# Optimization experiments

Hardware: AMD Instinct MI355X
Metric: run time of the kernel (lower is better)

## Reference

```python
import jax, jax.numpy as jnp
import numpy as np

H, DK, DV, BS = 8, 64, 64, 128


def setup_inputs() -> dict:
    key = jax.random.key(0)
    ks = jax.random.split(key, 6)
    B, T, D = 2, 8193, 1024
    inner = H * DK
    x = jax.random.normal(ks[0], (B, T, D), jnp.float32)
    s = 0.02
    Wq = jax.random.normal(ks[1], (D, inner), jnp.float32) * s
    Wk = jax.random.normal(ks[2], (D, inner), jnp.float32) * s
    Wv = jax.random.normal(ks[3], (D, H * DV), jnp.float32) * s
    Wo = jax.random.normal(ks[4], (H * DV, D), jnp.float32) * s
    bo = jnp.zeros((D,), jnp.float32)
    return {"x": x, "Wq": Wq, "Wk": Wk, "Wv": Wv, "Wo": Wo, "bo": bo}


def _bigbird(x, Wq, Wk, Wv, Wo, bo):
    B, T, D = x.shape
    N = T - 1
    nb = N // BS
    scale = 1.0 / jnp.sqrt(jnp.asarray(DK, x.dtype))
    # projections -> (B, H, T, d)
    q = (x @ Wq).reshape(B, T, H, DK).transpose(0, 2, 1, 3)
    k = (x @ Wk).reshape(B, T, H, DK).transpose(0, 2, 1, 3)
    v = (x @ Wv).reshape(B, T, H, DV).transpose(0, 2, 1, 3)

    # global token (position 0) attends to everything
    sg = jnp.einsum('bhd,bhtd->bht', q[:, :, 0], k) * scale
    pg = jax.nn.softmax(sg, axis=-1)
    out_g = jnp.einsum('bht,bhtd->bhd', pg, v)  # (B,H,DV)

    kg = k[:, :, 0]  # (B,H,DK)
    vg = v[:, :, 0]  # (B,H,DV)
    qx = q[:, :, 1:].reshape(B, H, nb, BS, DK)
    kx = k[:, :, 1:].reshape(B, H, nb, BS, DK)
    vx = v[:, :, 1:].reshape(B, H, nb, BS, DV)

    # zero-pad one block on each side (faithful to original: zero blocks, not masked)
    kp = jnp.pad(kx, ((0, 0), (0, 0), (1, 1), (0, 0), (0, 0)))
    vp = jnp.pad(vx, ((0, 0), (0, 0), (1, 1), (0, 0), (0, 0)))
    k_local = jnp.concatenate([kp[:, :, 0:nb], kp[:, :, 1:nb + 1], kp[:, :, 2:nb + 2]], axis=3)
    v_local = jnp.concatenate([vp[:, :, 0:nb], vp[:, :, 1:nb + 1], vp[:, :, 2:nb + 2]], axis=3)

    kg_e = jnp.broadcast_to(kg[:, :, None, None, :], (B, H, nb, 1, DK))
    vg_e = jnp.broadcast_to(vg[:, :, None, None, :], (B, H, nb, 1, DV))
    k_full = jnp.concatenate([kg_e, k_local], axis=3)  # (B,H,nb,1+3BS,DK)
    v_full = jnp.concatenate([vg_e, v_local], axis=3)

    scores = jnp.einsum('bhnqd,bhnkd->bhnqk', qx, k_full) * scale
    p = jax.nn.softmax(scores, axis=-1)
    out_x = jnp.einsum('bhnqk,bhnkd->bhnqd', p, v_full).reshape(B, H, N, DV)

    out = jnp.concatenate([out_g[:, :, None, :], out_x], axis=2)  # (B,H,T,DV)
    out = out.transpose(0, 2, 1, 3).reshape(B, T, H * DV)
    return out @ Wo + bo


def reference(x, Wq, Wk, Wv, Wo, bo):
    return _bigbird(x, Wq, Wk, Wv, Wo, bo)
```

## Files before the change

### kernel.cpp

```cpp
#include <hip/hip_runtime.h>
#include <hip/hip_bf16.h>

#define T_TOK 8193
#define MROWS 16386
#define NBLK  64
#define GCH   16
#define GCS   513

typedef __attribute__((ext_vector_type(8))) short bf16x8;
typedef __attribute__((ext_vector_type(4))) float f32x4;
typedef unsigned short u16;
typedef unsigned int   u32;

__device__ __forceinline__ float blo(u32 u){ return __uint_as_float(u << 16); }
__device__ __forceinline__ float bhi(u32 u){ return __uint_as_float(u & 0xffff0000u); }
__device__ __forceinline__ u16 f2b(float f){
  u32 u = __float_as_uint(f);
  u = (u + 0x7fffu + ((u >> 16) & 1u)) >> 16;
  return (u16)u;
}
__device__ __forceinline__ float b2f(u16 v){ return __uint_as_float(((u32)v) << 16); }

#define GLDS16(gsrc, ldst) \
  __builtin_amdgcn_global_load_lds((const __attribute__((address_space(1))) void*)(gsrc), \
                                   (__attribute__((address_space(3))) void*)(ldst), 16, 0, 0)

__global__ __launch_bounds__(256)
void convx(const float* __restrict__ x, u16* __restrict__ xb)
{
  const size_t i = (size_t)blockIdx.x * 256 + threadIdx.x;
  const float4* p = (const float4*)x + i * 2;
  float4 a = p[0], b = p[1];
  uint4 st;
  st.x = (u32)f2b(a.x) | ((u32)f2b(a.y) << 16);
  st.y = (u32)f2b(a.z) | ((u32)f2b(a.w) << 16);
  st.z = (u32)f2b(b.x) | ((u32)f2b(b.y) << 16);
  st.w = (u32)f2b(b.z) | ((u32)f2b(b.w) << 16);
  *(uint4*)(xb + i * 8) = st;
}

__global__ __launch_bounds__(256)
void transposeW(const float* __restrict__ B0, const float* __restrict__ B1,
                const float* __restrict__ B2, int bpart,
                u16* __restrict__ outT, int K)
{
  __shared__ float tile[64][65];
  const int n0 = blockIdx.x * 64;
  const int k0 = blockIdx.y * 64;
  const int tx = threadIdx.x & 63;
  const int ty = threadIdx.x >> 6;
  const int part = n0 / bpart;
  const float* Bm = part == 0 ? B0 : (part == 1 ? B1 : B2);
  const int bn = n0 - part * bpart;
  #pragma unroll
  for (int i = 0; i < 16; ++i) {
    int k = i * 4 + ty;
    tile[tx][k] = Bm[(size_t)(k0 + k) * bpart + bn + tx];
  }
  __syncthreads();
  #pragma unroll
  for (int i = 0; i < 16; ++i) {
    int r = i * 4 + ty;
    outT[(size_t)(n0 + r) * K + k0 + tx] = f2b(tile[r][tx]);
  }
}

template<bool OUT_F32>
__global__ __launch_bounds__(256)
void gemm_bf(const u16* __restrict__ A, const u16* __restrict__ BT,
             void* __restrict__ Cp, const float* __restrict__ bias,
             int M, int K, int ntm, int ntn, int ldc)
{
  __shared__ u16 As[128 * 32];
  __shared__ u16 Bs[128 * 32];
  const int tid  = threadIdx.x;
  const int lane = tid & 63;
  const int wid  = tid >> 6;
  const int l15  = lane & 15;
  const int g    = lane >> 4;
  const int wr   = (wid >> 1) * 64;
  const int wc   = (wid & 1) * 64;

  const int nwg  = gridDim.x;
  const int orig = blockIdx.x;
  const int q8 = nwg >> 3, r8 = nwg & 7;
  const int xcd = orig & 7, loc = orig >> 3;
  const int wg = (xcd < r8 ? xcd * (q8 + 1) : r8 * (q8 + 1) + (xcd - r8) * q8) + loc;
  const int GT  = 8;
  const int gsz = GT * ntn;
  const int tg  = wg / gsz;
  const int rem = wg - tg * gsz;
  const int gt  = (ntm - tg * GT < GT) ? (ntm - tg * GT) : GT;
  const int tn  = rem / gt;
  const int tml = rem - tn * gt;
  const int tm  = tg * GT + tml;
  const int bm0 = tm * 128, bn0 = tn * 128;

  f32x4 acc[4][4];
  #pragma unroll
  for (int i = 0; i < 4; ++i)
    #pragma unroll
    for (int j = 0; j < 4; ++j) { f32x4 z = {0.f,0.f,0.f,0.f}; acc[i][j] = z; }

  const int c0 = tid, c1 = tid + 256;
  int ar0 = bm0 + (c0 >> 2); if (ar0 >= M) ar0 = M - 1;
  int ar1 = bm0 + (c1 >> 2); if (ar1 >= M) ar1 = M - 1;
  const u16* Ag0 = A + (size_t)ar0 * K + (c0 & 3) * 8;
  const u16* Ag1 = A + (size_t)ar1 * K + (c1 & 3) * 8;
  const u16* Bg0 = BT + (size_t)(bn0 + (c0 >> 2)) * K + (c0 & 3) * 8;
  const u16* Bg1 = BT + (size_t)(bn0 + (c1 >> 2)) * K + (c1 & 3) * 8;
  u16* la0 = As + c0 * 8;  u16* la1 = As + c1 * 8;
  u16* lb0 = Bs + c0 * 8;  u16* lb1 = Bs + c1 * 8;

  for (int kt = 0; kt < K; kt += 32) {
    __syncthreads();
    GLDS16(Ag0 + kt, la0);
    GLDS16(Ag1 + kt, la1);
    GLDS16(Bg0 + kt, lb0);
    GLDS16(Bg1 + kt, lb1);
    __syncthreads();
    bf16x8 af[4], bfr[4];
    #pragma unroll
    for (int mi = 0; mi < 4; ++mi)
      af[mi] = *(const bf16x8*)&As[(wr + mi * 16 + l15) * 32 + g * 8];
    #pragma unroll
    for (int ni = 0; ni < 4; ++ni)
      bfr[ni] = *(const bf16x8*)&Bs[(wc + ni * 16 + l15) * 32 + g * 8];
    #pragma unroll
    for (int mi = 0; mi < 4; ++mi)
      #pragma unroll
      for (int ni = 0; ni < 4; ++ni)
        acc[mi][ni] = __builtin_amdgcn_mfma_f32_16x16x32_bf16(af[mi], bfr[ni], acc[mi][ni], 0, 0, 0);
  }

  const int r0 = g * 4;
  #pragma unroll
  for (int mi = 0; mi < 4; ++mi) {
    #pragma unroll
    for (int r = 0; r < 4; ++r) {
      int grow = bm0 + wr + mi * 16 + r0 + r;
      if (grow >= M) continue;
      #pragma unroll
      for (int ni = 0; ni < 4; ++ni) {
        int gcol  = bn0 + wc + ni * 16 + l15;
        float val = acc[mi][ni][r];
        if (OUT_F32) ((float*)Cp)[(size_t)grow * ldc + gcol] = val + bias[gcol];
        else         ((u16*)Cp)[(size_t)grow * ldc + gcol]   = f2b(val);
      }
    }
  }
}

__global__ __launch_bounds__(256)
void gsplit(const u16* __restrict__ qkv, float* __restrict__ gbuf)
{
  const int c   = blockIdx.x & 15;
  const int h   = (blockIdx.x >> 4) & 7;
  const int b   = blockIdx.x >> 7;
  const int tid = threadIdx.x;
  const int lane = tid & 63;
  const int wid  = tid >> 6;
  const int t0 = c * GCS;
  const int t1 = (t0 + GCS < T_TOK) ? (t0 + GCS) : T_TOK;
  const int nt = t1 - t0;

  __shared__ float sc[GCS];
  __shared__ float q0s[64];
  __shared__ float wredm[4], wreds[4];
  __shared__ float psum[4][64];

  const size_t base = (size_t)b * T_TOK * 1536;
  if (tid < 32) {
    u32 u = ((const u32*)(qkv + base + h * 64))[tid];
    q0s[2 * tid] = blo(u); q0s[2 * tid + 1] = bhi(u);
  }
  __syncthreads();

  float lmax = -INFINITY;
  for (int tt = tid; tt < nt; tt += 256) {
    const uint4* kp = (const uint4*)(qkv + base + (size_t)(t0 + tt) * 1536 + 512 + h * 64);
    float a = 0.f;
    #pragma unroll
    for (int q8 = 0; q8 < 8; ++q8) {
      uint4 kk = kp[q8];
      a += q0s[q8*8+0]*blo(kk.x) + q0s[q8*8+1]*bhi(kk.x)
         + q0s[q8*8+2]*blo(kk.y) + q0s[q8*8+3]*bhi(kk.y)
         + q0s[q8*8+4]*blo(kk.z) + q0s[q8*8+5]*bhi(kk.z)
         + q0s[q8*8+6]*blo(kk.w) + q0s[q8*8+7]*bhi(kk.w);
    }
    a *= 0.125f;
    sc[tt] = a;
    lmax = fmaxf(lmax, a);
  }
  for (int o = 32; o; o >>= 1) lmax = fmaxf(lmax, __shfl_xor(lmax, o, 64));
  if (lane == 0) wredm[wid] = lmax;
  __syncthreads();
  float bmax = fmaxf(fmaxf(wredm[0], wredm[1]), fmaxf(wredm[2], wredm[3]));
  float lsum = 0.f;
  for (int tt = tid; tt < nt; tt += 256) {
    float e = __expf(sc[tt] - bmax);
    sc[tt] = e;
    lsum += e;
  }
  for (int o = 32; o; o >>= 1) lsum += __shfl_xor(lsum, o, 64);
  if (lane == 0) wreds[wid] = lsum;
  __syncthreads();
  float bsum = wreds[0] + wreds[1] + wreds[2] + wreds[3];

  const int g = tid >> 6;
  const int d = tid & 63;
  float acc = 0.f;
  for (int tt = g; tt < nt; tt += 4)
    acc += sc[tt] * b2f(qkv[base + (size_t)(t0 + tt) * 1536 + 1024 + h * 64 + d]);
  psum[g][d] = acc;
  __syncthreads();

  float* rec = gbuf + ((size_t)(b * 8 + h) * GCH + c) * 66;
  if (tid < 64)
    rec[2 + tid] = psum[0][tid] + psum[1][tid] + psum[2][tid] + psum[3][tid];
  if (tid == 64) { rec[0] = bmax; rec[1] = bsum; }
}

__global__ __launch_bounds__(64)
void gmerge(const float* __restrict__ gbuf, u16* __restrict__ attnb)
{
  const int bh = blockIdx.x;
  const int d  = threadIdx.x;
  const float* recs = gbuf + (size_t)bh * GCH * 66;
  float m = -INFINITY;
  #pragma unroll
  for (int c = 0; c < GCH; ++c) m = fmaxf(m, recs[c * 66]);
  float l = 0.f, o = 0.f;
  #pragma unroll
  for (int c = 0; c < GCH; ++c) {
    float e = __expf(recs[c * 66] - m);
    l += recs[c * 66 + 1] * e;
    o += recs[c * 66 + 2 + d] * e;
  }
  const int b = bh >> 3, h = bh & 7;
  attnb[(size_t)b * T_TOK * 512 + h * 64 + d] = f2b(o / l);
}

__global__ __launch_bounds__(256)
void local_attn_mfma(const u16* __restrict__ qkv, u16* __restrict__ attnb)
{
  const int bid = blockIdx.x;
  const int n = bid & 63;
  const int h = (bid >> 6) & 7;
  const int b = bid >> 9;
  const int tid  = threadIdx.x;
  const int lane = tid & 63;
  const int wid  = tid >> 6;
  const int l15  = lane & 15;
  const int g    = lane >> 4;

  __shared__ u16 K_lds[128 * 72];
  __shared__ u16 V_T[64 * 136];
  __shared__ u16 P_lds[4][32 * 72];
  __shared__ float bb[4][2][32];
  __shared__ float Kg[64], Vg[64];

  const size_t rb = (size_t)b * T_TOK;
  if (tid < 64) {
    Kg[tid] = b2f(qkv[rb * 1536 + 512 + h * 64 + tid]);
    Vg[tid] = b2f(qkv[rb * 1536 + 1024 + h * 64 + tid]);
  }

  const int q0row = 1 + n * 128 + wid * 32;
  bf16x8 qf[2][2];
  #pragma unroll
  for (int qt = 0; qt < 2; ++qt)
    #pragma unroll
    for (int kk = 0; kk < 2; ++kk)
      qf[qt][kk] = *(const bf16x8*)(qkv + (rb + q0row + qt * 16 + l15) * 1536 + h * 64 + kk * 32 + g * 8);

  __syncthreads();

  float sg[2];
  #pragma unroll
  for (int qt = 0; qt < 2; ++qt) {
    float part = 0.f;
    #pragma unroll
    for (int kk = 0; kk < 2; ++kk)
      #pragma unroll
      for (int i = 0; i < 8; ++i)
        part += b2f((u16)qf[qt][kk][i]) * Kg[kk * 32 + g * 8 + i];
    part += __shfl_xor(part, 16, 64);
    part += __shfl_xor(part, 32, 64);
    sg[qt] = part * 0.125f;
  }

  float m[2] = {-INFINITY, -INFINITY};
  float l[2] = {0.f, 0.f};
  f32x4 of[2][4];
  #pragma unroll
  for (int qt = 0; qt < 2; ++qt)
    #pragma unroll
    for (int dt = 0; dt < 4; ++dt) { f32x4 z = {0.f,0.f,0.f,0.f}; of[qt][dt] = z; }

  for (int dblk = 0; dblk < 3; ++dblk) {
    const int blk = n + dblk - 1;
    if (blk < 0 || blk >= NBLK) continue;
    const size_t krow0 = rb + 1 + (size_t)blk * 128;

    __syncthreads();
    #pragma unroll
    for (int it = 0; it < 4; ++it) {
      int c = it * 256 + tid;
      int key = c >> 3, oct = c & 7;
      *(uint4*)&K_lds[key * 72 + oct * 8] =
          *(const uint4*)(qkv + (krow0 + key) * 1536 + 512 + h * 64 + oct * 8);
    }
    #pragma unroll
    for (int it = 0; it < 2; ++it) {
      int c = it * 256 + tid;
      int kp2 = c & 63, oct = c >> 6;
      const u16* s0 = qkv + (krow0 + 2 * kp2) * 1536 + 1024 + h * 64 + oct * 8;
      uint4 va = *(const uint4*)s0;
      uint4 vb4 = *(const uint4*)(s0 + 1536);
      union { uint4 q; u16 hh[8]; } ua, ub;
      ua.q = va; ub.q = vb4;
      #pragma unroll
      for (int i = 0; i < 8; ++i) {
        u32 w = (u32)ua.hh[i] | ((u32)ub.hh[i] << 16);
        *(u32*)&V_T[(oct * 8 + i) * 136 + 2 * kp2] = w;
      }
    }
    __syncthreads();

    f32x4 st[2][8];
    #pragma unroll
    for (int kt = 0; kt < 8; ++kt) {
      bf16x8 kfr[2];
      #pragma unroll
      for (int kk = 0; kk < 2; ++kk)
        kfr[kk] = *(const bf16x8*)&K_lds[(kt * 16 + l15) * 72 + kk * 32 + g * 8];
      #pragma unroll
      for (int qt = 0; qt < 2; ++qt) {
        f32x4 z = {0.f,0.f,0.f,0.f};
        z = __builtin_amdgcn_mfma_f32_16x16x32_bf16(kfr[0], qf[qt][0], z, 0, 0, 0);
        z = __builtin_amdgcn_mfma_f32_16x16x32_bf16(kfr[1], qf[qt][1], z, 0, 0, 0);
        st[qt][kt] = z;
      }
    }
    #pragma unroll
    for (int qt = 0; qt < 2; ++qt) {
      float bm = -INFINITY;
      #pragma unroll
      for (int kt = 0; kt < 8; ++kt)
        #pragma unroll
        for (int r = 0; r < 4; ++r) bm = fmaxf(bm, st[qt][kt][r]);
      bm = fmaxf(bm, __shfl_xor(bm, 16, 64));
      bm = fmaxf(bm, __shfl_xor(bm, 32, 64));
      bm *= 0.125f;
      float mn = fmaxf(m[qt], bm);
      float corr = __expf(m[qt] - mn);
      float bsum = 0.f;
      #pragma unroll
      for (int kt = 0; kt < 8; ++kt)
        #pragma unroll
        for (int r = 0; r < 4; ++r) {
          float p = __expf(__builtin_fmaf(st[qt][kt][r], 0.125f, -mn));
          st[qt][kt][r] = p;
          bsum += p;
        }
      bsum += __shfl_xor(bsum, 16, 64);
      bsum += __shfl_xor(bsum, 32, 64);
      l[qt] = l[qt] * corr + bsum;
      m[qt] = mn;
      if (lane < 16) bb[wid][0][qt * 16 + lane] = corr;
    }
    float rc[2][4];
    #pragma unroll
    for (int qt = 0; qt < 2; ++qt)
      #pragma unroll
      for (int r = 0; r < 4; ++r) rc[qt][r] = bb[wid][0][qt * 16 + g * 4 + r];
    #pragma unroll
    for (int qt = 0; qt < 2; ++qt)
      #pragma unroll
      for (int dt = 0; dt < 4; ++dt)
        #pragma unroll
        for (int r = 0; r < 4; ++r) of[qt][dt][r] *= rc[qt][r];

    u16* P_w = (u16*)P_lds[wid];
    #pragma unroll
    for (int half = 0; half < 2; ++half) {
      #pragma unroll
      for (int qt = 0; qt < 2; ++qt)
        #pragma unroll
        for (int k4 = 0; k4 < 4; ++k4) {
          int kt = half * 4 + k4;
          u16 h0 = f2b(st[qt][kt][0]), h1 = f2b(st[qt][kt][1]);
          u16 h2 = f2b(st[qt][kt][2]), h3 = f2b(st[qt][kt][3]);
          uint2 pk = { (u32)h0 | ((u32)h1 << 16), (u32)h2 | ((u32)h3 << 16) };
          *(uint2*)&P_w[(qt * 16 + l15) * 72 + k4 * 16 + g * 4] = pk;
        }
      #pragma unroll
      for (int ks = 0; ks < 2; ++ks) {
        bf16x8 pa[2];
        #pragma unroll
        for (int qt = 0; qt < 2; ++qt)
          pa[qt] = *(const bf16x8*)&P_w[(qt * 16 + l15) * 72 + ks * 32 + g * 8];
        #pragma unroll
        for (int dt = 0; dt < 4; ++dt) {
          bf16x8 vb = *(const bf16x8*)&V_T[(dt * 16 + l15) * 136 + half * 64 + ks * 32 + g * 8];
          #pragma unroll
          for (int qt = 0; qt < 2; ++qt)
            of[qt][dt] = __builtin_amdgcn_mfma_f32_16x16x32_bf16(pa[qt], vb, of[qt][dt], 0, 0, 0);
        }
      }
    }
  }

  const int nz = (n == 0) + (n == NBLK - 1);
  #pragma unroll
  for (int qt = 0; qt < 2; ++qt) {
    float mf   = fmaxf(m[qt], sg[qt]);
    float corr = __expf(m[qt] - mf);
    float eg   = __expf(sg[qt] - mf);
    float lf   = l[qt] * corr + eg;
    if (nz) lf += (float)(nz * 128) * __expf(-mf);
    float inv = 1.f / lf;
    if (lane < 16) {
      bb[wid][0][qt * 16 + lane] = corr * inv;
      bb[wid][1][qt * 16 + lane] = eg * inv;
    }
  }
  float vgr[4];
  #pragma unroll
  for (int dt = 0; dt < 4; ++dt) vgr[dt] = Vg[dt * 16 + l15];
  #pragma unroll
  for (int qt = 0; qt < 2; ++qt)
    #pragma unroll
    for (int r = 0; r < 4; ++r) {
      float af = bb[wid][0][qt * 16 + g * 4 + r];
      float bf = bb[wid][1][qt * 16 + g * 4 + r];
      int row = q0row + qt * 16 + g * 4 + r;
      u16* dst = attnb + (rb + row) * 512 + h * 64;
      #pragma unroll
      for (int dt = 0; dt < 4; ++dt)
        dst[dt * 16 + l15] = f2b(of[qt][dt][r] * af + bf * vgr[dt]);
    }
}

extern "C" void kernel_launch(void* const* d_in, const int* in_sizes, int n_in,
                              void* d_out, int out_size, void* d_ws, size_t ws_size,
                              hipStream_t stream) {
  (void)in_sizes; (void)n_in; (void)out_size; (void)ws_size;
  const float* x  = (const float*)d_in[0];
  const float* Wq = (const float*)d_in[1];
  const float* Wk = (const float*)d_in[2];
  const float* Wv = (const float*)d_in[3];
  const float* Wo = (const float*)d_in[4];
  const float* bo = (const float*)d_in[5];
  float* out = (float*)d_out;

  char* ws = (char*)d_ws;
  u16* qkv   = (u16*)ws;
  u16* xb    = (u16*)(ws + 50337792);
  u16* attnb = (u16*)(ws + 50337792);
  u16* WoT   = (u16*)(ws + 67117056);
  u16* WqkvT = (u16*)d_out;
  float* gbuf = (float*)((char*)d_out + (4 << 20));

  dim3 blk(256);
  convx<<<dim3(8193), blk, 0, stream>>>(x, xb);
  transposeW<<<dim3(24, 16), blk, 0, stream>>>(Wq, Wk, Wv, 512, WqkvT, 1024);
  gemm_bf<false><<<dim3(129 * 12), blk, 0, stream>>>(xb, WqkvT, qkv, nullptr, MROWS, 1024, 129, 12, 1536);
  transposeW<<<dim3(16, 8), blk, 0, stream>>>(Wo, Wo, Wo, 1024, WoT, 512);
  gsplit<<<dim3(256), blk, 0, stream>>>(qkv, gbuf);
  gmerge<<<dim3(16), dim3(64), 0, stream>>>(gbuf, attnb);
  local_attn_mfma<<<dim3(1024), blk, 0, stream>>>(qkv, attnb);
  gemm_bf<true><<<dim3(129 * 8), blk, 0, stream>>>(attnb, WoT, out, bo, MROWS, 512, 129, 8, 1024);
}
```

Measured before the change: 227.7 us.

## Triple-buffer GEMM LDS tiles with async prefetch and XOR-swizzled layout

The bf16 GEMM main loop now uses three LDS buffers and prefetches tiles two steps ahead with global_load_lds, waiting on vmcnt counts instead of a full sync after each load. This overlaps global-to-LDS traffic with the MFMA work. It also XOR-swizzles the 16-byte chunk positions in LDS so fragment reads hit fewer bank conflicts. In exchange it triples LDS use per block, which may lower occupancy, and the hand-written vmcnt waits depend on the exact number of outstanding loads.

Result: faster. 217.7 us (-4.4%).

```diff
diff --git a/kernel.cpp b/kernel.cpp
--- a/kernel.cpp
+++ b/kernel.cpp
@@ -71,8 +71,8 @@
              void* __restrict__ Cp, const float* __restrict__ bias,
              int M, int K, int ntm, int ntn, int ldc)
 {
-  __shared__ u16 As[128 * 32];
-  __shared__ u16 Bs[128 * 32];
+  __shared__ u16 As[3][128 * 32];
+  __shared__ u16 Bs[3][128 * 32];
   const int tid  = threadIdx.x;
   const int lane = tid & 63;
   const int wid  = tid >> 6;
@@ -102,36 +102,57 @@
     #pragma unroll
     for (int j = 0; j < 4; ++j) { f32x4 z = {0.f,0.f,0.f,0.f}; acc[i][j] = z; }
 
-  const int c0 = tid, c1 = tid + 256;
-  int ar0 = bm0 + (c0 >> 2); if (ar0 >= M) ar0 = M - 1;
-  int ar1 = bm0 + (c1 >> 2); if (ar1 >= M) ar1 = M - 1;
-  const u16* Ag0 = A + (size_t)ar0 * K + (c0 & 3) * 8;
-  const u16* Ag1 = A + (size_t)ar1 * K + (c1 & 3) * 8;
-  const u16* Bg0 = BT + (size_t)(bn0 + (c0 >> 2)) * K + (c0 & 3) * 8;
-  const u16* Bg1 = BT + (size_t)(bn0 + (c1 >> 2)) * K + (c1 & 3) * 8;
-  u16* la0 = As + c0 * 8;  u16* la1 = As + c1 * 8;
-  u16* lb0 = Bs + c0 * 8;  u16* lb1 = Bs + c1 * 8;
-
-  for (int kt = 0; kt < K; kt += 32) {
-    __syncthreads();
-    GLDS16(Ag0 + kt, la0);
-    GLDS16(Ag1 + kt, la1);
-    GLDS16(Bg0 + kt, lb0);
-    GLDS16(Bg1 + kt, lb1);
-    __syncthreads();
+  const int srcq = ((tid & 3) ^ ((tid >> 3) & 3)) * 8;
+  int ar0 = bm0 + (tid >> 2);      if (ar0 >= M) ar0 = M - 1;
+  int ar1 = bm0 + 64 + (tid >> 2); if (ar1 >= M) ar1 = M - 1;
+  const u16* Ag0 = A + (size_t)ar0 * K + srcq;
+  const u16* Ag1 = A + (size_t)ar1 * K + srcq;
+  const u16* Bg0 = BT + (size_t)(bn0 + (tid >> 2)) * K + srcq;
+  const u16* Bg1 = BT + (size_t)(bn0 + 64 + (tid >> 2)) * K + srcq;
+  const int ld0 = tid * 8, ld1 = tid * 8 + 2048;
+
+#define STAGE_T(bf, kt) do { \
+    GLDS16(Ag0 + (kt), &As[bf][ld0]); \
+    GLDS16(Ag1 + (kt), &As[bf][ld1]); \
+    GLDS16(Bg0 + (kt), &Bs[bf][ld0]); \
+    GLDS16(Bg1 + (kt), &Bs[bf][ld1]); \
+  } while (0)
+
+  const int Tst = K >> 5;
+  STAGE_T(0, 0);
+  STAGE_T(1, 32);
+
+  const int qa = (g ^ ((l15 >> 1) & 3)) * 8;
+
+  int cur = 0;
+  for (int t = 0; t < Tst; ++t) {
+    __builtin_amdgcn_s_barrier();
+    int nb = cur + 2; if (nb >= 3) nb -= 3;
+    if (t + 2 < Tst) {
+      STAGE_T(nb, (t + 2) * 32);
+      asm volatile("s_waitcnt vmcnt(8)" ::: "memory");
+    } else if (t + 2 == Tst) {
+      asm volatile("s_waitcnt vmcnt(4)" ::: "memory");
+    } else {
+      asm volatile("s_waitcnt vmcnt(0)" ::: "memory");
+    }
+    __builtin_amdgcn_s_barrier();
+    __builtin_amdgcn_sched_barrier(0);
     bf16x8 af[4], bfr[4];
     #pragma unroll
     for (int mi = 0; mi < 4; ++mi)
-      af[mi] = *(const bf16x8*)&As[(wr + mi * 16 + l15) * 32 + g * 8];
+      af[mi] = *(const bf16x8*)&As[cur][(wr + mi * 16 + l15) * 32 + qa];
     #pragma unroll
     for (int ni = 0; ni < 4; ++ni)
-      bfr[ni] = *(const bf16x8*)&Bs[(wc + ni * 16 + l15) * 32 + g * 8];
+      bfr[ni] = *(const bf16x8*)&Bs[cur][(wc + ni * 16 + l15) * 32 + qa];
     #pragma unroll
     for (int mi = 0; mi < 4; ++mi)
       #pragma unroll
       for (int ni = 0; ni < 4; ++ni)
         acc[mi][ni] = __builtin_amdgcn_mfma_f32_16x16x32_bf16(af[mi], bfr[ni], acc[mi][ni], 0, 0, 0);
-  }
+    cur = (cur + 1 == 3) ? 0 : cur + 1;
+  }
+#undef STAGE_T
 
   const int r0 = g * 4;
   #pragma unroll
```

## Replace GEMM with 256x256-tile, 8-wave, double-buffered, swizzled-LDS pipelined kernel

Applied to the files above, without the earlier changes.

Replaces the simple 128x128 single-buffered bf16 GEMM with a 256x256-tile kernel using 8 waves and a 128 KB double-buffered LDS ring. The LDS layout is XOR-swizzled, and loads for future k-slices are interleaved with MFMA phases using explicit vmcnt waits, barriers and setprio. The aim is to hide global-load latency and improve data reuse in both the QKV and output projections. In exchange it uses far more LDS and registers, and the grid has fewer workgroups (390 and 260), which risks tail imbalance.

Measured after the change: 205.1 us. -9.9%, faster.

```diff
diff --git a/kernel.cpp b/kernel.cpp
--- a/kernel.cpp
+++ b/kernel.cpp
@@ -66,79 +66,133 @@
 }
 
 template<bool OUT_F32>
-__global__ __launch_bounds__(256)
-void gemm_bf(const u16* __restrict__ A, const u16* __restrict__ BT,
-             void* __restrict__ Cp, const float* __restrict__ bias,
-             int M, int K, int ntm, int ntn, int ldc)
+__global__ __launch_bounds__(512, 2)
+void gemm8(const u16* __restrict__ A, const u16* __restrict__ BT,
+           void* __restrict__ Cp, const float* __restrict__ bias,
+           int M, int K, int ntm, int ntn, int ldc)
 {
-  __shared__ u16 As[128 * 32];
-  __shared__ u16 Bs[128 * 32];
+  __shared__ u16 lds[65536];
   const int tid  = threadIdx.x;
   const int lane = tid & 63;
   const int wid  = tid >> 6;
   const int l15  = lane & 15;
   const int g    = lane >> 4;
-  const int wr   = (wid >> 1) * 64;
-  const int wc   = (wid & 1) * 64;
+  const int wrh  = wid >> 2;
+  const int wc   = (wid & 3) * 64;
+  const int bh   = (wid & 3) >> 1;
+  const int wcl  = (wid & 1) * 64;
 
   const int nwg  = gridDim.x;
   const int orig = blockIdx.x;
   const int q8 = nwg >> 3, r8 = nwg & 7;
   const int xcd = orig & 7, loc = orig >> 3;
   const int wg = (xcd < r8 ? xcd * (q8 + 1) : r8 * (q8 + 1) + (xcd - r8) * q8) + loc;
-  const int GT  = 8;
+  const int GT  = 4;
   const int gsz = GT * ntn;
   const int tg  = wg / gsz;
   const int rem = wg - tg * gsz;
   const int gt  = (ntm - tg * GT < GT) ? (ntm - tg * GT) : GT;
   const int tn  = rem / gt;
   const int tml = rem - tn * gt;
-  const int tm  = tg * GT + tml;
-  const int bm0 = tm * 128, bn0 = tn * 128;
-
-  f32x4 acc[4][4];
-  #pragma unroll
-  for (int i = 0; i < 4; ++i)
+  const int bm0 = (tg * GT + tml) * 256;
+  const int bn0 = tn * 256;
+
+  f32x4 acc[8][4];
+  #pragma unroll
+  for (int i = 0; i < 8; ++i)
     #pragma unroll
     for (int j = 0; j < 4; ++j) { f32x4 z = {0.f,0.f,0.f,0.f}; acc[i][j] = z; }
 
-  const int c0 = tid, c1 = tid + 256;
-  int ar0 = bm0 + (c0 >> 2); if (ar0 >= M) ar0 = M - 1;
-  int ar1 = bm0 + (c1 >> 2); if (ar1 >= M) ar1 = M - 1;
-  const u16* Ag0 = A + (size_t)ar0 * K + (c0 & 3) * 8;
-  const u16* Ag1 = A + (size_t)ar1 * K + (c1 & 3) * 8;
-  const u16* Bg0 = BT + (size_t)(bn0 + (c0 >> 2)) * K + (c0 & 3) * 8;
-  const u16* Bg1 = BT + (size_t)(bn0 + (c1 >> 2)) * K + (c1 & 3) * 8;
-  u16* la0 = As + c0 * 8;  u16* la1 = As + c1 * 8;
-  u16* lb0 = Bs + c0 * 8;  u16* lb1 = Bs + c1 * 8;
-
-  for (int kt = 0; kt < K; kt += 32) {
-    __syncthreads();
-    GLDS16(Ag0 + kt, la0);
-    GLDS16(Ag1 + kt, la1);
-    GLDS16(Bg0 + kt, lb0);
-    GLDS16(Bg1 + kt, lb1);
-    __syncthreads();
-    bf16x8 af[4], bfr[4];
-    #pragma unroll
-    for (int mi = 0; mi < 4; ++mi)
-      af[mi] = *(const bf16x8*)&As[(wr + mi * 16 + l15) * 32 + g * 8];
-    #pragma unroll
-    for (int ni = 0; ni < 4; ++ni)
-      bfr[ni] = *(const bf16x8*)&Bs[(wc + ni * 16 + l15) * 32 + g * 8];
-    #pragma unroll
-    for (int mi = 0; mi < 4; ++mi)
-      #pragma unroll
-      for (int ni = 0; ni < 4; ++ni)
-        acc[mi][ni] = __builtin_amdgcn_mfma_f32_16x16x32_bf16(af[mi], bfr[ni], acc[mi][ni], 0, 0, 0);
-  }
-
-  const int r0 = g * 4;
-  #pragma unroll
-  for (int mi = 0; mi < 4; ++mi) {
+  const int rr  = tid >> 3;
+  const int gq  = (((tid & 7) ^ (rr & 7))) * 8;
+  const int ldst0 = tid * 8;
+  u32 aOff[2][2], bOff[2][2];
+  #pragma unroll
+  for (int h = 0; h < 2; ++h)
+    #pragma unroll
+    for (int j = 0; j < 2; ++j) {
+      int ar = bm0 + h * 128 + j * 64 + rr; if (ar >= M) ar = M - 1;
+      aOff[h][j] = (u32)ar * (u32)K + gq;
+      bOff[h][j] = (u32)(bn0 + h * 128 + j * 64 + rr) * (u32)K + gq;
+    }
+
+#define LBASE(BUF, AB, H) (((((BUF)*2 + (AB))*2 + (H)) * 8192))
+#define STAGE_A(BUF, H, KO) do { \
+    GLDS16(A + aOff[H][0] + (KO), &lds[LBASE(BUF,0,H) + ldst0]); \
+    GLDS16(A + aOff[H][1] + (KO), &lds[LBASE(BUF,0,H) + 4096 + ldst0]); \
+  } while (0)
+#define STAGE_B(BUF, H, KO) do { \
+    GLDS16(BT + bOff[H][0] + (KO), &lds[LBASE(BUF,1,H) + ldst0]); \
+    GLDS16(BT + bOff[H][1] + (KO), &lds[LBASE(BUF,1,H) + 4096 + ldst0]); \
+  } while (0)
+
+  int ca[2];
+  ca[0] = ((0 * 4 + g) ^ (l15 & 7)) * 8;
+  ca[1] = ((1 * 4 + g) ^ (l15 & 7)) * 8;
+
+  bf16x8 bf[4][2];
+
+#define PHASE(BUF, P, STAGE_STMT, DOVM, VMLAST) do { \
+    bf16x8 af[2][2]; \
+    if ((P) == 0) { \
+      _Pragma("unroll") \
+      for (int ni = 0; ni < 4; ++ni) { \
+        bf[ni][0] = *(const bf16x8*)&lds[LBASE(BUF,1,bh) + (wcl + ni*16 + l15)*64 + ca[0]]; \
+        bf[ni][1] = *(const bf16x8*)&lds[LBASE(BUF,1,bh) + (wcl + ni*16 + l15)*64 + ca[1]]; \
+      } \
+    } \
+    _Pragma("unroll") \
+    for (int mi = 0; mi < 2; ++mi) { \
+      af[mi][0] = *(const bf16x8*)&lds[LBASE(BUF,0,wrh) + (((P)*2+mi)*16 + l15)*64 + ca[0]]; \
+      af[mi][1] = *(const bf16x8*)&lds[LBASE(BUF,0,wrh) + (((P)*2+mi)*16 + l15)*64 + ca[1]]; \
+    } \
+    STAGE_STMT; \
+    __builtin_amdgcn_s_barrier(); \
+    __builtin_amdgcn_s_setprio(1); \
+    _Pragma("unroll") \
+    for (int mi = 0; mi < 2; ++mi) \
+      _Pragma("unroll") \
+      for (int ni = 0; ni < 4; ++ni) { \
+        acc[(P)*2+mi][ni] = __builtin_amdgcn_mfma_f32_16x16x32_bf16(af[mi][0], bf[ni][0], acc[(P)*2+mi][ni], 0, 0, 0); \
+        acc[(P)*2+mi][ni] = __builtin_amdgcn_mfma_f32_16x16x32_bf16(af[mi][1], bf[ni][1], acc[(P)*2+mi][ni], 0, 0, 0); \
+      } \
+    __builtin_amdgcn_s_setprio(0); \
+    if (DOVM) { \
+      if (VMLAST) asm volatile("s_waitcnt vmcnt(0)" ::: "memory"); \
+      else        asm volatile("s_waitcnt vmcnt(4)" ::: "memory"); \
+    } \
+    __builtin_amdgcn_s_barrier(); \
+  } while (0)
+
+  STAGE_B(0, 0, 0);  STAGE_B(0, 1, 0);
+  STAGE_A(0, 0, 0);  STAGE_A(0, 1, 0);
+  STAGE_B(1, 0, 64); STAGE_B(1, 1, 64);
+  asm volatile("s_waitcnt vmcnt(4)" ::: "memory");
+  __builtin_amdgcn_s_barrier();
+
+  const int nit = K >> 7;
+  for (int it = 0; it < nit; ++it) {
+    const int t2 = it << 7;
+    const bool ls = (it == nit - 1);
+    PHASE(0, 0, STAGE_A(1, 0, t2 + 64), false, false);
+    PHASE(0, 1, STAGE_A(1, 1, t2 + 64), false, false);
+    PHASE(0, 2, if (!ls) STAGE_B(0, 0, t2 + 128), false, false);
+    PHASE(0, 3, if (!ls) STAGE_B(0, 1, t2 + 128), true, ls);
+    PHASE(1, 0, if (!ls) STAGE_A(0, 0, t2 + 128), false, false);
+    PHASE(1, 1, if (!ls) STAGE_A(0, 1, t2 + 128), false, false);
+    PHASE(1, 2, if (!ls) STAGE_B(1, 0, t2 + 192), false, false);
+    PHASE(1, 3, if (!ls) STAGE_B(1, 1, t2 + 192), true, ls);
+  }
+#undef PHASE
+#undef STAGE_A
+#undef STAGE_B
+#undef LBASE
+
+  #pragma unroll
+  for (int mi = 0; mi < 8; ++mi) {
     #pragma unroll
     for (int r = 0; r < 4; ++r) {
-      int grow = bm0 + wr + mi * 16 + r0 + r;
+      int grow = bm0 + wrh * 128 + mi * 16 + g * 4 + r;
       if (grow >= M) continue;
       #pragma unroll
       for (int ni = 0; ni < 4; ++ni) {
@@ -466,10 +520,10 @@
   dim3 blk(256);
   convx<<<dim3(8193), blk, 0, stream>>>(x, xb);
   transposeW<<<dim3(24, 16), blk, 0, stream>>>(Wq, Wk, Wv, 512, WqkvT, 1024);
-  gemm_bf<false><<<dim3(129 * 12), blk, 0, stream>>>(xb, WqkvT, qkv, nullptr, MROWS, 1024, 129, 12, 1536);
+  gemm8<false><<<dim3(65 * 6), dim3(512), 0, stream>>>(xb, WqkvT, qkv, nullptr, MROWS, 1024, 65, 6, 1536);
   transposeW<<<dim3(16, 8), blk, 0, stream>>>(Wo, Wo, Wo, 1024, WoT, 512);
   gsplit<<<dim3(256), blk, 0, stream>>>(qkv, gbuf);
   gmerge<<<dim3(16), dim3(64), 0, stream>>>(gbuf, attnb);
   local_attn_mfma<<<dim3(1024), blk, 0, stream>>>(qkv, attnb);
-  gemm_bf<true><<<dim3(129 * 8), blk, 0, stream>>>(attnb, WoT, out, bo, MROWS, 512, 129, 8, 1024);
-}
+  gemm8<true><<<dim3(65 * 4), dim3(512), 0, stream>>>(attnb, WoT, out, bo, MROWS, 512, 65, 4, 1024);
+}
```

## Rewrite bf16 GEMM with triple-buffered LDS pipeline, 256x128 tiles, swizzle

Applied to the files above, without the earlier changes.

Replaces the GEMM with a 512-thread kernel computing 256x128 output tiles. The K dimension is streamed through a three-stage LDS ring buffer with async global-to-LDS loads issued two steps ahead, plus an XOR swizzle to avoid LDS bank conflicts. The MFMA loop is split into two halves with s_setprio and barriers to interleave LDS reads and compute. This aims to hide global load latency and raise MFMA utilisation, at the cost of more LDS per block, fewer blocks in the grid, and more barriers.

Result: faster. 203.1 us (median of 2 runs) (-10.8%).

```diff
diff --git a/kernel.cpp b/kernel.cpp
--- a/kernel.cpp
+++ b/kernel.cpp
@@ -66,35 +66,34 @@
 }
 
 template<bool OUT_F32>
-__global__ __launch_bounds__(256)
-void gemm_bf(const u16* __restrict__ A, const u16* __restrict__ BT,
-             void* __restrict__ Cp, const float* __restrict__ bias,
-             int M, int K, int ntm, int ntn, int ldc)
+__global__ __launch_bounds__(512, 4)
+void gemmk(const u16* __restrict__ A, const u16* __restrict__ BT,
+           void* __restrict__ Cp, const float* __restrict__ bias,
+           int M, int K, int ntm, int ntn, int ldc)
 {
-  __shared__ u16 As[128 * 32];
-  __shared__ u16 Bs[128 * 32];
+  __shared__ u16 lds[36864];
   const int tid  = threadIdx.x;
   const int lane = tid & 63;
   const int wid  = tid >> 6;
   const int l15  = lane & 15;
   const int g    = lane >> 4;
-  const int wr   = (wid >> 1) * 64;
-  const int wc   = (wid & 1) * 64;
+  const int wm   = (wid >> 1) * 64;
+  const int wn   = (wid & 1) * 64;
 
   const int nwg  = gridDim.x;
   const int orig = blockIdx.x;
   const int q8 = nwg >> 3, r8 = nwg & 7;
   const int xcd = orig & 7, loc = orig >> 3;
   const int wg = (xcd < r8 ? xcd * (q8 + 1) : r8 * (q8 + 1) + (xcd - r8) * q8) + loc;
-  const int GT  = 8;
+  const int GT  = 4;
   const int gsz = GT * ntn;
   const int tg  = wg / gsz;
   const int rem = wg - tg * gsz;
   const int gt  = (ntm - tg * GT < GT) ? (ntm - tg * GT) : GT;
   const int tn  = rem / gt;
   const int tml = rem - tn * gt;
-  const int tm  = tg * GT + tml;
-  const int bm0 = tm * 128, bn0 = tn * 128;
+  const int bm0 = (tg * GT + tml) * 256;
+  const int bn0 = tn * 128;
 
   f32x4 acc[4][4];
   #pragma unroll
@@ -102,47 +101,77 @@
     #pragma unroll
     for (int j = 0; j < 4; ++j) { f32x4 z = {0.f,0.f,0.f,0.f}; acc[i][j] = z; }
 
-  const int c0 = tid, c1 = tid + 256;
-  int ar0 = bm0 + (c0 >> 2); if (ar0 >= M) ar0 = M - 1;
-  int ar1 = bm0 + (c1 >> 2); if (ar1 >= M) ar1 = M - 1;
-  const u16* Ag0 = A + (size_t)ar0 * K + (c0 & 3) * 8;
-  const u16* Ag1 = A + (size_t)ar1 * K + (c1 & 3) * 8;
-  const u16* Bg0 = BT + (size_t)(bn0 + (c0 >> 2)) * K + (c0 & 3) * 8;
-  const u16* Bg1 = BT + (size_t)(bn0 + (c1 >> 2)) * K + (c1 & 3) * 8;
-  u16* la0 = As + c0 * 8;  u16* la1 = As + c1 * 8;
-  u16* lb0 = Bs + c0 * 8;  u16* lb1 = Bs + c1 * 8;
-
-  for (int kt = 0; kt < K; kt += 32) {
-    __syncthreads();
-    GLDS16(Ag0 + kt, la0);
-    GLDS16(Ag1 + kt, la1);
-    GLDS16(Bg0 + kt, lb0);
-    GLDS16(Bg1 + kt, lb1);
-    __syncthreads();
-    bf16x8 af[4], bfr[4];
-    #pragma unroll
-    for (int mi = 0; mi < 4; ++mi)
-      af[mi] = *(const bf16x8*)&As[(wr + mi * 16 + l15) * 32 + g * 8];
+  const int rr   = tid >> 2;
+  const int ch   = tid & 3;
+  const int srcq = (ch ^ ((rr >> 1) & 3)) * 8;
+  int ar0 = bm0 + rr;        if (ar0 >= M) ar0 = M - 1;
+  int ar1 = bm0 + 128 + rr;  if (ar1 >= M) ar1 = M - 1;
+  const u32 aOff0 = (u32)ar0 * (u32)K + srcq;
+  const u32 aOff1 = (u32)ar1 * (u32)K + srcq;
+  const u32 bOff  = (u32)(bn0 + rr) * (u32)K + srcq;
+  const int ld8   = tid * 8;
+
+#define STG(BUF, KO) do { \
+    GLDS16(A + aOff0 + (KO), &lds[(BUF) * 12288 + ld8]); \
+    GLDS16(A + aOff1 + (KO), &lds[(BUF) * 12288 + 4096 + ld8]); \
+    GLDS16(BT + bOff + (KO), &lds[(BUF) * 12288 + 8192 + ld8]); \
+  } while (0)
+
+  const int ca = (g ^ ((l15 >> 1) & 3)) * 8;
+
+  STG(0, 0);
+  STG(1, 32);
+  asm volatile("s_waitcnt vmcnt(3)" ::: "memory");
+  __builtin_amdgcn_s_barrier();
+
+  const int nt = K >> 5;
+  int bufc = 0, bufn = 2;
+  for (int t = 0; t < nt; ++t) {
+    const int base = bufc * 12288;
+    const bool more = (t + 2 < nt);
+    bf16x8 bfr[4], af[2];
     #pragma unroll
     for (int ni = 0; ni < 4; ++ni)
-      bfr[ni] = *(const bf16x8*)&Bs[(wc + ni * 16 + l15) * 32 + g * 8];
-    #pragma unroll
-    for (int mi = 0; mi < 4; ++mi)
+      bfr[ni] = *(const bf16x8*)&lds[base + 8192 + (wn + ni * 16 + l15) * 32 + ca];
+    af[0] = *(const bf16x8*)&lds[base + (wm + l15) * 32 + ca];
+    af[1] = *(const bf16x8*)&lds[base + (wm + 16 + l15) * 32 + ca];
+    if (more) STG(bufn, (t + 2) * 32);
+    __builtin_amdgcn_s_barrier();
+    __builtin_amdgcn_s_setprio(1);
+    #pragma unroll
+    for (int mi = 0; mi < 2; ++mi)
       #pragma unroll
       for (int ni = 0; ni < 4; ++ni)
         acc[mi][ni] = __builtin_amdgcn_mfma_f32_16x16x32_bf16(af[mi], bfr[ni], acc[mi][ni], 0, 0, 0);
-  }
-
-  const int r0 = g * 4;
+    __builtin_amdgcn_s_setprio(0);
+    __builtin_amdgcn_s_barrier();
+    af[0] = *(const bf16x8*)&lds[base + (wm + 32 + l15) * 32 + ca];
+    af[1] = *(const bf16x8*)&lds[base + (wm + 48 + l15) * 32 + ca];
+    __builtin_amdgcn_s_barrier();
+    __builtin_amdgcn_s_setprio(1);
+    #pragma unroll
+    for (int mi = 0; mi < 2; ++mi)
+      #pragma unroll
+      for (int ni = 0; ni < 4; ++ni)
+        acc[2 + mi][ni] = __builtin_amdgcn_mfma_f32_16x16x32_bf16(af[mi], bfr[ni], acc[2 + mi][ni], 0, 0, 0);
+    __builtin_amdgcn_s_setprio(0);
+    if (more) asm volatile("s_waitcnt vmcnt(3)" ::: "memory");
+    else      asm volatile("s_waitcnt vmcnt(0)" ::: "memory");
+    __builtin_amdgcn_s_barrier();
+    bufc = (bufc + 1 == 3) ? 0 : bufc + 1;
+    bufn = (bufn + 1 == 3) ? 0 : bufn + 1;
+  }
+#undef STG
+
   #pragma unroll
   for (int mi = 0; mi < 4; ++mi) {
     #pragma unroll
     for (int r = 0; r < 4; ++r) {
-      int grow = bm0 + wr + mi * 16 + r0 + r;
+      int grow = bm0 + wm + mi * 16 + g * 4 + r;
       if (grow >= M) continue;
       #pragma unroll
       for (int ni = 0; ni < 4; ++ni) {
-        int gcol  = bn0 + wc + ni * 16 + l15;
+        int gcol  = bn0 + wn + ni * 16 + l15;
         float val = acc[mi][ni][r];
         if (OUT_F32) ((float*)Cp)[(size_t)grow * ldc + gcol] = val + bias[gcol];
         else         ((u16*)Cp)[(size_t)grow * ldc + gcol]   = f2b(val);
@@ -466,10 +495,10 @@
   dim3 blk(256);
   convx<<<dim3(8193), blk, 0, stream>>>(x, xb);
   transposeW<<<dim3(24, 16), blk, 0, stream>>>(Wq, Wk, Wv, 512, WqkvT, 1024);
-  gemm_bf<false><<<dim3(129 * 12), blk, 0, stream>>>(xb, WqkvT, qkv, nullptr, MROWS, 1024, 129, 12, 1536);
+  gemmk<false><<<dim3(65 * 12), dim3(512), 0, stream>>>(xb, WqkvT, qkv, nullptr, MROWS, 1024, 65, 12, 1536);
   transposeW<<<dim3(16, 8), blk, 0, stream>>>(Wo, Wo, Wo, 1024, WoT, 512);
   gsplit<<<dim3(256), blk, 0, stream>>>(qkv, gbuf);
   gmerge<<<dim3(16), dim3(64), 0, stream>>>(gbuf, attnb);
   local_attn_mfma<<<dim3(1024), blk, 0, stream>>>(qkv, attnb);
-  gemm_bf<true><<<dim3(129 * 8), blk, 0, stream>>>(attnb, WoT, out, bo, MROWS, 512, 129, 8, 1024);
-}
+  gemmk<true><<<dim3(65 * 8), dim3(512), 0, stream>>>(attnb, WoT, out, bo, MROWS, 512, 65, 8, 1024);
+}
```
